# Performance work log

Measured on AMD Instinct MI355X. Metric: run time of the kernel, lower is better.

The kernel has to match this reference:

```python
import jax, jax.numpy as jnp
import numpy as np

B, T, D = 2, 2048, 2048   # batch, seq, model dim
H = 1408                  # expert hidden dim
E = 16                    # routed experts
S = 2                     # shared experts
TOP_K = 2
SCALE = 0.02


def setup_inputs() -> dict:
    key = jax.random.key(0)
    ks = jax.random.split(key, 6)
    return {
        "x": jax.random.normal(ks[0], (B, T, D), jnp.float32),
        "gate_w": jax.random.normal(ks[1], (D, E), jnp.float32) * SCALE,
        "shared_w1": jax.random.normal(ks[2], (S, D, H), jnp.float32) * SCALE,
        "shared_w2": jax.random.normal(ks[3], (S, H, D), jnp.float32) * SCALE,
        "expert_w1": jax.random.normal(ks[4], (E, D, H), jnp.float32) * SCALE,
        "expert_w2": jax.random.normal(ks[5], (E, H, D), jnp.float32) * SCALE,
    }


def reference(x, gate_w, shared_w1, shared_w2, expert_w1, expert_w2):
    xf = x.reshape(-1, x.shape[-1])            # [T_tot, D]
    n_tok = xf.shape[0]

    # shared experts: sum of SiLU FFNs
    sh = jax.nn.silu(jnp.einsum('td,sdh->sth', xf, shared_w1))
    shared_out = jnp.einsum('sth,shd->td', sh, shared_w2)

    # router
    logits = xf @ gate_w                       # [T_tot, E]
    probs = jax.nn.softmax(logits, axis=-1)
    topk_w, topk_idx = jax.lax.top_k(probs, TOP_K)
    topk_w = topk_w / topk_w.sum(axis=-1, keepdims=True)

    # aux load-balancing loss
    aux_loss = (probs.mean(axis=0) * logits.mean(axis=0)).sum() * E

    # scatter normalized top-k weights into dense [T_tot, E] combine matrix
    combine = jnp.zeros((n_tok, E), xf.dtype).at[
        jnp.arange(n_tok)[:, None], topk_idx
    ].add(topk_w)

    # routed experts computed densely over all tokens, combined by routing weights
    h = jax.nn.silu(jnp.einsum('td,edh->eth', xf, expert_w1))   # [E, T_tot, H]
    eo = jnp.einsum('eth,ehd->etd', h, expert_w2)               # [E, T_tot, D]
    routed_out = jnp.einsum('te,etd->td', combine, eo)

    total = (shared_out + routed_out).reshape(x.shape)
    return total, aux_loss
```

## Files before the change

kernel.cpp:

```cpp
#include <hip/hip_runtime.h>
#include <hip/hip_bf16.h>


#define T_TOT   4096
#define DMODEL  2048
#define HDIM    1408
#define NEXP    16
#define MAXSLOT 10240
#define MAXTILE 80
#define RBLK    512

typedef short     bf16x8_t  __attribute__((ext_vector_type(8)));
typedef float     f32x4_t   __attribute__((ext_vector_type(4)));
typedef ushort    u16x8_t   __attribute__((ext_vector_type(8)));

__device__ __forceinline__ ushort f2bf(float f) {
    unsigned u = __float_as_uint(f);
    u += 0x7fffu + ((u >> 16) & 1u);
    return (ushort)(u >> 16);
}
__device__ __forceinline__ float bf2f(ushort b) { return __uint_as_float((unsigned)b << 16); }
__device__ __forceinline__ float silu(float v) { return v / (1.0f + __expf(-v)); }

__device__ __forceinline__ void async16(const ushort* g, ushort* l) {
    __builtin_amdgcn_global_load_lds((const __attribute__((address_space(1))) void*)g,
                                     (__attribute__((address_space(3))) void*)l, 16, 0, 0);
}


union SMem {
    struct {
        float  sred[4][2][16][17];
        double sp[4][2][NEXP];
        double sl[4][2][NEXP];
    } r;
    ushort t[64][72];
};

__device__ __forceinline__ void transpose_tile(SMem& sm, int id,
        const float* __restrict__ src, ushort* __restrict__ dst,
        int C, long sbatch, long dbatch, int ldd, int TX, int TY) {
    int z = id / (TX * TY); int rem = id - z * TX * TY;
    int bx = rem % TX, by = rem / TX;
    const float* s = src + (long)z * sbatch;
    ushort* d = dst + (long)z * dbatch;
    int c0 = bx * 64, r0 = by * 64;
    int tx = threadIdx.x & 15, ty = threadIdx.x >> 4;
#pragma unroll
    for (int i = 0; i < 4; i++) {
        int r = ty + i * 16;
        float4 v = *(const float4*)(s + (size_t)(r0 + r) * C + c0 + tx * 4);
        ushort4 o; o.x = f2bf(v.x); o.y = f2bf(v.y); o.z = f2bf(v.z); o.w = f2bf(v.w);
        *(ushort4*)&sm.t[r][tx * 4] = o;
    }
    __syncthreads();
    int cx = threadIdx.x & 7, cy = threadIdx.x >> 3;
#pragma unroll
    for (int i = 0; i < 2; i++) {
        int cc = cy + i * 32;
        u16x8_t o;
#pragma unroll
        for (int j = 0; j < 8; j++) o[j] = sm.t[cx * 8 + j][cc];
        *(u16x8_t*)(d + (size_t)(c0 + cc) * ldd + r0 + cx * 8) = o;
    }
}

__device__ __forceinline__ void router_block(SMem& sm, int bid,
        const float* __restrict__ x, const float* __restrict__ gw, ushort* __restrict__ xbuf,
        int* __restrict__ topk_idx, float* __restrict__ topk_w,
        double* __restrict__ pparts, double* __restrict__ lparts) {
    const int wv = threadIdx.x >> 6, l = threadIdx.x & 63;
    const int tBase = bid * 8 + wv * 2;

    float acc0[NEXP], acc1[NEXP];
#pragma unroll
    for (int e = 0; e < NEXP; e++) { acc0[e] = 0.f; acc1[e] = 0.f; }

    const float* x0 = x + (size_t)tBase * DMODEL;
    const float* x1 = x0 + DMODEL;
    ushort* xo0 = xbuf + (size_t)tBase * DMODEL;
    ushort* xo1 = xo0 + DMODEL;

#pragma unroll
    for (int i = 0; i < 8; i++) {
        const int d0 = i * 256 + l * 4;
        float4 xa = *(const float4*)(x0 + d0);
        float4 xb4 = *(const float4*)(x1 + d0);
        ushort4 oa; oa.x = f2bf(xa.x); oa.y = f2bf(xa.y); oa.z = f2bf(xa.z); oa.w = f2bf(xa.w);
        ushort4 ob; ob.x = f2bf(xb4.x); ob.y = f2bf(xb4.y); ob.z = f2bf(xb4.z); ob.w = f2bf(xb4.w);
        *(ushort4*)(xo0 + d0) = oa;
        *(ushort4*)(xo1 + d0) = ob;
        const float xs0[4] = {xa.x, xa.y, xa.z, xa.w};
        const float xs1[4] = {xb4.x, xb4.y, xb4.z, xb4.w};
#pragma unroll
        for (int r = 0; r < 4; r++) {
            const float4* g = (const float4*)(gw + (size_t)(d0 + r) * NEXP);
            float4 q0 = g[0], q1 = g[1], q2 = g[2], q3 = g[3];
            const float gf[16] = {q0.x, q0.y, q0.z, q0.w, q1.x, q1.y, q1.z, q1.w,
                                  q2.x, q2.y, q2.z, q2.w, q3.x, q3.y, q3.z, q3.w};
#pragma unroll
            for (int e = 0; e < NEXP; e++) {
                acc0[e] += xs0[r] * gf[e];
                acc1[e] += xs1[r] * gf[e];
            }
        }
    }

#pragma unroll
    for (int e = 0; e < NEXP; e++) {
        acc0[e] += __shfl_xor(acc0[e], 32); acc0[e] += __shfl_xor(acc0[e], 16);
        acc1[e] += __shfl_xor(acc1[e], 32); acc1[e] += __shfl_xor(acc1[e], 16);
    }

    if (l < 16) {
#pragma unroll
        for (int e = 0; e < NEXP; e++) { sm.r.sred[wv][0][l][e] = acc0[e]; sm.r.sred[wv][1][l][e] = acc1[e]; }
    }
    __syncthreads();

    if (l < 32) {
        const int tok = l >> 4, e = l & 15;
        double lg = 0.0;
#pragma unroll
        for (int g = 0; g < 16; g++) lg += (double)sm.r.sred[wv][tok][g][e];

        double m = lg;
#pragma unroll
        for (int off = 8; off; off >>= 1) { double o = __shfl_xor(m, off); m = o > m ? o : m; }
        double pe = exp(lg - m);
        double ss = pe;
#pragma unroll
        for (int off = 8; off; off >>= 1) ss += __shfl_xor(ss, off);
        double p = pe / ss;

        double v = p; int ie = e;
#pragma unroll
        for (int off = 8; off; off >>= 1) {
            double ov = __shfl_xor(v, off); int oi = __shfl_xor(ie, off);
            if (ov > v || (ov == v && oi < ie)) { v = ov; ie = oi; }
        }
        double v2 = (e == ie) ? -1.0 : p; int ie2 = e;
#pragma unroll
        for (int off = 8; off; off >>= 1) {
            double ov = __shfl_xor(v2, off); int oi = __shfl_xor(ie2, off);
            if (ov > v2 || (ov == v2 && oi < ie2)) { v2 = ov; ie2 = oi; }
        }

        sm.r.sp[wv][tok][e] = p; sm.r.sl[wv][tok][e] = lg;

        if (e == 0) {
            int t = tBase + tok;
            double s2 = v + v2;
            topk_idx[t * 2] = ie;  topk_idx[t * 2 + 1] = ie2;
            topk_w[t * 2] = (float)(v / s2); topk_w[t * 2 + 1] = (float)(v2 / s2);
        }
    }
    __syncthreads();

    if (threadIdx.x < NEXP) {
        int e = threadIdx.x;
        double ps = 0.0, ls = 0.0;
#pragma unroll
        for (int w = 0; w < 4; w++) { ps += sm.r.sp[w][0][e] + sm.r.sp[w][1][e]; ls += sm.r.sl[w][0][e] + sm.r.sl[w][1][e]; }
        pparts[bid * NEXP + e] = ps;
        lparts[bid * NEXP + e] = ls;
    }
}

#define PB0 RBLK
#define PB1 (PB0 + 1408)
#define PB2 (PB1 + 1408)
#define PB3 (PB2 + 11264)
#define PB4 (PB3 + 11264)

__global__ __launch_bounds__(256) void prep_kernel(
        const float* __restrict__ x, const float* __restrict__ gw,
        const float* __restrict__ sw1, const float* __restrict__ sw2,
        const float* __restrict__ ew1, const float* __restrict__ ew2,
        ushort* __restrict__ xb, ushort* __restrict__ w1t, ushort* __restrict__ w2t,
        ushort* __restrict__ ew1t, ushort* __restrict__ ew2t,
        int* __restrict__ topk_idx, float* __restrict__ topk_w,
        double* __restrict__ pparts, double* __restrict__ lparts) {
    __shared__ SMem sm;
    int bid = blockIdx.x;
    if (bid < PB0) {
        router_block(sm, bid, x, gw, xb, topk_idx, topk_w, pparts, lparts);
    } else if (bid < PB1) {
        transpose_tile(sm, bid - PB0, sw1, w1t, HDIM, (long)DMODEL * HDIM, (long)HDIM * DMODEL,
                       DMODEL, HDIM / 64, DMODEL / 64);
    } else if (bid < PB2) {
        transpose_tile(sm, bid - PB1, sw2, w2t, DMODEL, (long)HDIM * DMODEL, (long)HDIM,
                       2 * HDIM, DMODEL / 64, HDIM / 64);
    } else if (bid < PB3) {
        transpose_tile(sm, bid - PB2, ew1, ew1t, HDIM, (long)DMODEL * HDIM, (long)HDIM * DMODEL,
                       DMODEL, HDIM / 64, DMODEL / 64);
    } else {
        transpose_tile(sm, bid - PB3, ew2, ew2t, DMODEL, (long)HDIM * DMODEL, (long)DMODEL * HDIM,
                       HDIM, DMODEL / 64, HDIM / 64);
    }
}


__global__ __launch_bounds__(1024) void plan_kernel(
        const int* __restrict__ topk_idx, const float* __restrict__ topk_w,
        const double* __restrict__ pparts, const double* __restrict__ lparts,
        int* __restrict__ tile_expert, int* __restrict__ tile_row, int* __restrict__ meta,
        int* __restrict__ slot_token, float* __restrict__ slot_w, int* __restrict__ slot_of,
        float* __restrict__ out_aux) {
    __shared__ int hist[NEXP];
    __shared__ int curs[NEXP];
    __shared__ double pred[32][NEXP], lred[32][NEXP];
    __shared__ double paux[NEXP], laux[NEXP];
    const int tid = threadIdx.x;
    if (tid < NEXP) hist[tid] = 0;
    __syncthreads();
    for (int i = tid; i < T_TOT * 2; i += 1024) atomicAdd(&hist[topk_idx[i]], 1);
    for (int i = tid; i < MAXSLOT; i += 1024) { slot_token[i] = 0; slot_w[i] = 0.0f; }
    if (tid < 512) {
        int e = tid & 15, c = tid >> 4;
        double ps = 0.0, ls = 0.0;
        for (int b = c * 16; b < c * 16 + 16; b++) { ps += pparts[b * NEXP + e]; ls += lparts[b * NEXP + e]; }
        pred[c][e] = ps; lred[c][e] = ls;
    }
    __syncthreads();
    if (tid < NEXP) {
        double ps = 0.0, ls = 0.0;
        for (int c = 0; c < 32; c++) { ps += pred[c][tid]; ls += lred[c][tid]; }
        paux[tid] = ps; laux[tid] = ls;
    }
    __syncthreads();
    if (tid == 0) {
        int off = 0, nt = 0;
        for (int e = 0; e < NEXP; e++) {
            curs[e] = off;
            int tiles = (hist[e] + 127) >> 7;
            for (int j = 0; j < tiles; j++) { tile_expert[nt] = e; tile_row[nt] = off + j * 128; nt++; }
            off += tiles * 128;
        }
        meta[0] = nt; meta[1] = off;
        double aux = 0.0;
        for (int e = 0; e < NEXP; e++)
            aux += (paux[e] / (double)T_TOT) * (laux[e] / (double)T_TOT);
        out_aux[0] = (float)(aux * (double)NEXP);
    }
    __syncthreads();
    for (int i = tid; i < T_TOT * 2; i += 1024) {
        int e = topk_idx[i];
        int pos = atomicAdd(&curs[e], 1);
        slot_token[pos] = i >> 1;
        slot_w[pos] = topk_w[i];
        slot_of[i] = pos;
    }
}


template<bool INDIRECT_A>
__device__ __forceinline__ void gemm_tile_core(const ushort* __restrict__ A, const ushort* __restrict__ B,
                                               int lda, int ldb, int K, int m0, int n0,
                                               const int* __restrict__ rowmap,
                                               f32x4_t acc[4][4], ushort* lds) {
    const int tid = threadIdx.x;
    const int w = tid >> 6, l = tid & 63;
    const int c0 = w * 2, c1 = c0 + 1;
    const int subrow = l >> 2;
    const int kc = (l & 3) * 8;
    int ar0 = c0 * 16 + subrow, ar1 = c1 * 16 + subrow;
    long ga0, ga1;
    if (INDIRECT_A) { ga0 = (long)rowmap[m0 + ar0]; ga1 = (long)rowmap[m0 + ar1]; }
    else            { ga0 = (long)(m0 + ar0);       ga1 = (long)(m0 + ar1); }
    const ushort* pa0 = A + ga0 * lda + kc;
    const ushort* pa1 = A + ga1 * lda + kc;
    const ushort* pb0 = B + (long)(n0 + ar0) * ldb + kc;
    const ushort* pb1 = B + (long)(n0 + ar1) * ldb + kc;
    const int wm = w & 1, wn = w >> 1;
    const int lrow = l & 15, quad = l >> 4;

    {
        ushort* d0 = lds + c0 * 512;
        ushort* d1 = lds + c1 * 512;
        async16(pa0, d0); async16(pa1, d1);
        async16(pb0, d0 + 4096); async16(pb1, d1 + 4096);
    }
    int cur = 0;
    for (int kt = 0; kt < K; kt += 32) {
        __syncthreads();
        if (kt + 32 < K) {
            pa0 += 32; pa1 += 32; pb0 += 32; pb1 += 32;
            ushort* e0 = lds + (cur ^ 1) * 8192 + c0 * 512;
            ushort* e1 = lds + (cur ^ 1) * 8192 + c1 * 512;
            async16(pa0, e0); async16(pa1, e1);
            async16(pb0, e0 + 4096); async16(pb1, e1 + 4096);
        }
        const ushort* As = lds + cur * 8192;
        const ushort* Bs = As + 4096;
        bf16x8_t a[4], b[4];
#pragma unroll
        for (int mi = 0; mi < 4; mi++)
            a[mi] = *(const bf16x8_t*)(As + (wm * 64 + mi * 16 + lrow) * 32 + quad * 8);
#pragma unroll
        for (int ni = 0; ni < 4; ni++)
            b[ni] = *(const bf16x8_t*)(Bs + (wn * 64 + ni * 16 + lrow) * 32 + quad * 8);
#pragma unroll
        for (int mi = 0; mi < 4; mi++)
#pragma unroll
            for (int ni = 0; ni < 4; ni++)
                acc[mi][ni] = __builtin_amdgcn_mfma_f32_16x16x32_bf16(a[mi], b[ni], acc[mi][ni], 0, 0, 0);
        cur ^= 1;
    }
}

__global__ __launch_bounds__(256, 3) void gemm_p1(const ushort* __restrict__ xb,
        const ushort* __restrict__ w1t, const ushort* __restrict__ ew1t,
        ushort* __restrict__ h, ushort* __restrict__ hg,
        const int* __restrict__ tile_expert, const int* __restrict__ tile_row,
        const int* __restrict__ meta, const int* __restrict__ slot_token) {
    __shared__ ushort lds[16384];
    f32x4_t acc[4][4];
#pragma unroll
    for (int mi = 0; mi < 4; mi++)
#pragma unroll
        for (int ni = 0; ni < 4; ni++) acc[mi][ni] = (f32x4_t){0.f, 0.f, 0.f, 0.f};

    const int bid = blockIdx.x;
    ushort* C; int ldc, m0, n0, colBase;
    if (bid < 704) {
        int z = bid / 352, rem = bid % 352;
        m0 = (rem % 32) * 128; n0 = (rem / 32) * 128;
        gemm_tile_core<false>(xb, w1t + (long)z * HDIM * DMODEL, DMODEL, DMODEL, DMODEL,
                              m0, n0, nullptr, acc, lds);
        C = h; ldc = 2 * HDIM; colBase = z * HDIM + n0;
    } else {
        int r = bid - 704;
        int tile = r % MAXTILE; n0 = (r / MAXTILE) * 128;
        if (tile >= meta[0]) return;
        int e = tile_expert[tile]; m0 = tile_row[tile];
        gemm_tile_core<true>(xb, ew1t + (long)e * HDIM * DMODEL, DMODEL, DMODEL, DMODEL,
                             m0, n0, slot_token, acc, lds);
        C = hg; ldc = HDIM; colBase = n0;
    }

    const int w = threadIdx.x >> 6, l = threadIdx.x & 63;
    const int wm = w & 1, wn = w >> 1, quad = l >> 4, lcol = l & 15;
#pragma unroll
    for (int mi = 0; mi < 4; mi++) {
        int rowb = m0 + wm * 64 + mi * 16 + quad * 4;
#pragma unroll
        for (int ni = 0; ni < 4; ni++) {
            int col = colBase + wn * 64 + ni * 16 + lcol;
#pragma unroll
            for (int r = 0; r < 4; r++)
                C[(long)(rowb + r) * ldc + col] = f2bf(silu(acc[mi][ni][r]));
        }
    }
}

__global__ __launch_bounds__(256, 3) void gemm_p2(const ushort* __restrict__ h,
        const ushort* __restrict__ w2t, const ushort* __restrict__ hg, const ushort* __restrict__ ew2t,
        float* __restrict__ out, ushort* __restrict__ ro,
        const int* __restrict__ tile_expert, const int* __restrict__ tile_row,
        const int* __restrict__ meta, const float* __restrict__ slot_w) {
    __shared__ ushort lds[16384];
    f32x4_t acc[4][4];
#pragma unroll
    for (int mi = 0; mi < 4; mi++)
#pragma unroll
        for (int ni = 0; ni < 4; ni++) acc[mi][ni] = (f32x4_t){0.f, 0.f, 0.f, 0.f};

    const int bid = blockIdx.x;
    const int w = threadIdx.x >> 6, l = threadIdx.x & 63;
    const int wm = w & 1, wn = w >> 1, quad = l >> 4, lcol = l & 15;

    if (bid < 512) {
        int m0 = (bid % 32) * 128, n0 = (bid / 32) * 128;
        gemm_tile_core<false>(h, w2t, 2 * HDIM, 2 * HDIM, 2 * HDIM, m0, n0, nullptr, acc, lds);
#pragma unroll
        for (int mi = 0; mi < 4; mi++) {
            int rowb = m0 + wm * 64 + mi * 16 + quad * 4;
#pragma unroll
            for (int ni = 0; ni < 4; ni++) {
                int col = n0 + wn * 64 + ni * 16 + lcol;
#pragma unroll
                for (int r = 0; r < 4; r++)
                    out[(long)(rowb + r) * DMODEL + col] = acc[mi][ni][r];
            }
        }
    } else {
        int r0 = bid - 512;
        int tile = r0 % MAXTILE; int n0 = (r0 / MAXTILE) * 128;
        if (tile >= meta[0]) return;
        int e = tile_expert[tile]; int m0 = tile_row[tile];
        gemm_tile_core<false>(hg, ew2t + (long)e * DMODEL * HDIM, HDIM, HDIM, HDIM,
                              m0, n0, nullptr, acc, lds);
#pragma unroll
        for (int mi = 0; mi < 4; mi++) {
            int rowb = m0 + wm * 64 + mi * 16 + quad * 4;
#pragma unroll
            for (int ni = 0; ni < 4; ni++) {
                int col = n0 + wn * 64 + ni * 16 + lcol;
#pragma unroll
                for (int r = 0; r < 4; r++) {
                    int row = rowb + r;
                    ro[(long)row * DMODEL + col] = f2bf(acc[mi][ni][r] * slot_w[row]);
                }
            }
        }
    }
}

__global__ __launch_bounds__(256) void combine_kernel(float* __restrict__ out, const ushort* __restrict__ ro,
                                                      const int* __restrict__ slot_of) {
    int t = blockIdx.x;
    int s1 = slot_of[t * 2], s2 = slot_of[t * 2 + 1];
    const u16x8_t* r1 = (const u16x8_t*)(ro + (size_t)s1 * DMODEL);
    const u16x8_t* r2 = (const u16x8_t*)(ro + (size_t)s2 * DMODEL);
    int i = threadIdx.x;
    u16x8_t a = r1[i], b = r2[i];
    float4* o = (float4*)(out + (size_t)t * DMODEL) + i * 2;
    float4 o0 = o[0], o1 = o[1];
    o0.x += bf2f(a[0]) + bf2f(b[0]); o0.y += bf2f(a[1]) + bf2f(b[1]);
    o0.z += bf2f(a[2]) + bf2f(b[2]); o0.w += bf2f(a[3]) + bf2f(b[3]);
    o1.x += bf2f(a[4]) + bf2f(b[4]); o1.y += bf2f(a[5]) + bf2f(b[5]);
    o1.z += bf2f(a[6]) + bf2f(b[6]); o1.w += bf2f(a[7]) + bf2f(b[7]);
    o[0] = o0; o[1] = o1;
}


extern "C" void kernel_launch(void* const* d_in, const int* in_sizes, int n_in,
                              void* d_out, int out_size, void* d_ws, size_t ws_size,
                              hipStream_t stream) {
    const float* x   = (const float*)d_in[0];
    const float* gw  = (const float*)d_in[1];
    const float* sw1 = (const float*)d_in[2];
    const float* sw2 = (const float*)d_in[3];
    const float* ew1 = (const float*)d_in[4];
    const float* ew2 = (const float*)d_in[5];
    float* out = (float*)d_out;

    char* p = (char*)d_ws;
    auto alloc = [&](size_t bytes) { char* r = p; p += (bytes + 511) & ~(size_t)511; return r; };
    ushort* xb    = (ushort*)alloc((size_t)T_TOT * DMODEL * 2);
    ushort* w1t   = (ushort*)alloc((size_t)2 * HDIM * DMODEL * 2);
    ushort* w2t   = (ushort*)alloc((size_t)DMODEL * 2 * HDIM * 2);
    ushort* ew1t  = (ushort*)alloc((size_t)NEXP * HDIM * DMODEL * 2);
    ushort* ew2t  = (ushort*)alloc((size_t)NEXP * DMODEL * HDIM * 2);
    ushort* h     = (ushort*)alloc((size_t)T_TOT * 2 * HDIM * 2);
    ushort* hg    = (ushort*)alloc((size_t)MAXSLOT * HDIM * 2);
    ushort* ro    = (ushort*)alloc((size_t)MAXSLOT * DMODEL * 2);
    int*    slot_token = (int*)alloc(MAXSLOT * 4);
    float*  slot_w     = (float*)alloc(MAXSLOT * 4);
    int*    slot_of    = (int*)alloc(T_TOT * 2 * 4);
    int*    topk_idx   = (int*)alloc(T_TOT * 2 * 4);
    float*  topk_w     = (float*)alloc(T_TOT * 2 * 4);
    int*    tile_expert= (int*)alloc(512);
    int*    tile_row   = (int*)alloc(512);
    int*    meta       = (int*)alloc(64);
    double* pparts     = (double*)alloc((size_t)RBLK * NEXP * 8);
    double* lparts     = (double*)alloc((size_t)RBLK * NEXP * 8);

    prep_kernel<<<PB4, 256, 0, stream>>>(x, gw, sw1, sw2, ew1, ew2,
                                         xb, w1t, w2t, ew1t, ew2t,
                                         topk_idx, topk_w, pparts, lparts);
    plan_kernel<<<1, 1024, 0, stream>>>(topk_idx, topk_w, pparts, lparts,
                                        tile_expert, tile_row, meta,
                                        slot_token, slot_w, slot_of, out + (size_t)T_TOT * DMODEL);
    gemm_p1<<<704 + MAXTILE * (HDIM / 128), 256, 0, stream>>>(
        xb, w1t, ew1t, h, hg, tile_expert, tile_row, meta, slot_token);
    gemm_p2<<<512 + MAXTILE * (DMODEL / 128), 256, 0, stream>>>(
        h, w2t, hg, ew2t, out, ro, tile_expert, tile_row, meta, slot_w);
    combine_kernel<<<T_TOT, 256, 0, stream>>>(out, ro, slot_of);
}
```

Before: 811.0 us.

## Transpose weights through registers and remap GEMM blocks across XCDs

```diff
diff --git a/kernel.cpp b/kernel.cpp
--- a/kernel.cpp
+++ b/kernel.cpp
@@ -27,17 +27,20 @@
                                      (__attribute__((address_space(3))) void*)l, 16, 0, 0);
 }
 
-
-union SMem {
-    struct {
-        float  sred[4][2][16][17];
-        double sp[4][2][NEXP];
-        double sl[4][2][NEXP];
-    } r;
-    ushort t[64][72];
+__device__ __forceinline__ int xcd_swz(int bid, int nwg) {
+    int q = nwg >> 3, r = nwg & 7;
+    int x = bid & 7, i = bid >> 3;
+    return (x < r ? x * (q + 1) : r * (q + 1) + (x - r) * q) + i;
+}
+
+
+struct SMem {
+    float  sred[4][2][16][17];
+    double sp[4][2][NEXP];
+    double sl[4][2][NEXP];
 };
 
-__device__ __forceinline__ void transpose_tile(SMem& sm, int id,
+__device__ __forceinline__ void transpose_reg(int id,
         const float* __restrict__ src, ushort* __restrict__ dst,
         int C, long sbatch, long dbatch, int ldd, int TX, int TY) {
     int z = id / (TX * TY); int rem = id - z * TX * TY;
@@ -45,24 +48,27 @@
     const float* s = src + (long)z * sbatch;
     ushort* d = dst + (long)z * dbatch;
     int c0 = bx * 64, r0 = by * 64;
-    int tx = threadIdx.x & 15, ty = threadIdx.x >> 4;
-#pragma unroll
-    for (int i = 0; i < 4; i++) {
-        int r = ty + i * 16;
-        float4 v = *(const float4*)(s + (size_t)(r0 + r) * C + c0 + tx * 4);
-        ushort4 o; o.x = f2bf(v.x); o.y = f2bf(v.y); o.z = f2bf(v.z); o.w = f2bf(v.w);
-        *(ushort4*)&sm.t[r][tx * 4] = o;
-    }
-    __syncthreads();
-    int cx = threadIdx.x & 7, cy = threadIdx.x >> 3;
-#pragma unroll
-    for (int i = 0; i < 2; i++) {
-        int cc = cy + i * 32;
-        u16x8_t o;
-#pragma unroll
-        for (int j = 0; j < 8; j++) o[j] = sm.t[cx * 8 + j][cc];
-        *(u16x8_t*)(d + (size_t)(c0 + cc) * ldd + r0 + cx * 8) = o;
-    }
+    const int w = threadIdx.x >> 6, lane = threadIdx.x & 63;
+    const int g = lane >> 4, s16 = lane & 15;
+    const int cw = w * 16 + g * 4;
+    const int rw = s16 * 4;
+
+    const float* sp = s + (size_t)(r0 + rw) * C + c0 + cw;
+    float4 v0 = *(const float4*)(sp);
+    float4 v1 = *(const float4*)(sp + C);
+    float4 v2 = *(const float4*)(sp + 2 * (size_t)C);
+    float4 v3 = *(const float4*)(sp + 3 * (size_t)C);
+
+    ushort* dp = d + (size_t)(c0 + cw) * ldd + r0 + rw;
+    ushort4 o;
+    o.x = f2bf(v0.x); o.y = f2bf(v1.x); o.z = f2bf(v2.x); o.w = f2bf(v3.x);
+    *(ushort4*)(dp) = o;
+    o.x = f2bf(v0.y); o.y = f2bf(v1.y); o.z = f2bf(v2.y); o.w = f2bf(v3.y);
+    *(ushort4*)(dp + ldd) = o;
+    o.x = f2bf(v0.z); o.y = f2bf(v1.z); o.z = f2bf(v2.z); o.w = f2bf(v3.z);
+    *(ushort4*)(dp + 2 * (size_t)ldd) = o;
+    o.x = f2bf(v0.w); o.y = f2bf(v1.w); o.z = f2bf(v2.w); o.w = f2bf(v3.w);
+    *(ushort4*)(dp + 3 * (size_t)ldd) = o;
 }
 
 __device__ __forceinline__ void router_block(SMem& sm, int bid,
@@ -114,7 +120,7 @@
 
     if (l < 16) {
 #pragma unroll
-        for (int e = 0; e < NEXP; e++) { sm.r.sred[wv][0][l][e] = acc0[e]; sm.r.sred[wv][1][l][e] = acc1[e]; }
+        for (int e = 0; e < NEXP; e++) { sm.sred[wv][0][l][e] = acc0[e]; sm.sred[wv][1][l][e] = acc1[e]; }
     }
     __syncthreads();
 
@@ -122,7 +128,7 @@
         const int tok = l >> 4, e = l & 15;
         double lg = 0.0;
 #pragma unroll
-        for (int g = 0; g < 16; g++) lg += (double)sm.r.sred[wv][tok][g][e];
+        for (int g = 0; g < 16; g++) lg += (double)sm.sred[wv][tok][g][e];
 
         double m = lg;
 #pragma unroll
@@ -146,7 +152,7 @@
             if (ov > v2 || (ov == v2 && oi < ie2)) { v2 = ov; ie2 = oi; }
         }
 
-        sm.r.sp[wv][tok][e] = p; sm.r.sl[wv][tok][e] = lg;
+        sm.sp[wv][tok][e] = p; sm.sl[wv][tok][e] = lg;
 
         if (e == 0) {
             int t = tBase + tok;
@@ -161,7 +167,7 @@
         int e = threadIdx.x;
         double ps = 0.0, ls = 0.0;
 #pragma unroll
-        for (int w = 0; w < 4; w++) { ps += sm.r.sp[w][0][e] + sm.r.sp[w][1][e]; ls += sm.r.sl[w][0][e] + sm.r.sl[w][1][e]; }
+        for (int w = 0; w < 4; w++) { ps += sm.sp[w][0][e] + sm.sp[w][1][e]; ls += sm.sl[w][0][e] + sm.sl[w][1][e]; }
         pparts[bid * NEXP + e] = ps;
         lparts[bid * NEXP + e] = ls;
     }
@@ -186,17 +192,17 @@
     if (bid < PB0) {
         router_block(sm, bid, x, gw, xb, topk_idx, topk_w, pparts, lparts);
     } else if (bid < PB1) {
-        transpose_tile(sm, bid - PB0, sw1, w1t, HDIM, (long)DMODEL * HDIM, (long)HDIM * DMODEL,
-                       DMODEL, HDIM / 64, DMODEL / 64);
+        transpose_reg(bid - PB0, sw1, w1t, HDIM, (long)DMODEL * HDIM, (long)HDIM * DMODEL,
+                      DMODEL, HDIM / 64, DMODEL / 64);
     } else if (bid < PB2) {
-        transpose_tile(sm, bid - PB1, sw2, w2t, DMODEL, (long)HDIM * DMODEL, (long)HDIM,
-                       2 * HDIM, DMODEL / 64, HDIM / 64);
+        transpose_reg(bid - PB1, sw2, w2t, DMODEL, (long)HDIM * DMODEL, (long)HDIM,
+                      2 * HDIM, DMODEL / 64, HDIM / 64);
     } else if (bid < PB3) {
-        transpose_tile(sm, bid - PB2, ew1, ew1t, HDIM, (long)DMODEL * HDIM, (long)HDIM * DMODEL,
-                       DMODEL, HDIM / 64, DMODEL / 64);
+        transpose_reg(bid - PB2, ew1, ew1t, HDIM, (long)DMODEL * HDIM, (long)HDIM * DMODEL,
+                      DMODEL, HDIM / 64, DMODEL / 64);
     } else {
-        transpose_tile(sm, bid - PB3, ew2, ew2t, DMODEL, (long)HDIM * DMODEL, (long)DMODEL * HDIM,
-                       HDIM, DMODEL / 64, HDIM / 64);
+        transpose_reg(bid - PB3, ew2, ew2t, DMODEL, (long)HDIM * DMODEL, (long)DMODEL * HDIM,
+                      HDIM, DMODEL / 64, HDIM / 64);
     }
 }
 
@@ -321,7 +327,9 @@
 #pragma unroll
         for (int ni = 0; ni < 4; ni++) acc[mi][ni] = (f32x4_t){0.f, 0.f, 0.f, 0.f};
 
-    const int bid = blockIdx.x;
+    int bid = blockIdx.x;
+    bid = (bid < 704) ? xcd_swz(bid, 704) : 704 + xcd_swz(bid - 704, MAXTILE * (HDIM / 128));
+
     ushort* C; int ldc, m0, n0, colBase;
     if (bid < 704) {
         int z = bid / 352, rem = bid % 352;
@@ -366,7 +374,9 @@
 #pragma unroll
         for (int ni = 0; ni < 4; ni++) acc[mi][ni] = (f32x4_t){0.f, 0.f, 0.f, 0.f};
 
-    const int bid = blockIdx.x;
+    int bid = blockIdx.x;
+    bid = (bid < 512) ? xcd_swz(bid, 512) : 512 + xcd_swz(bid - 512, MAXTILE * (DMODEL / 128));
+
     const int w = threadIdx.x >> 6, l = threadIdx.x & 63;
     const int wm = w & 1, wn = w >> 1, quad = l >> 4, lcol = l & 15;
 
```

Result: no change. 814.9 us (+0.5%).
